# Kernel optimization log

Measured on AMD Instinct MI355X. Metric: run time of the kernel, lower is better.

The kernel has to match this reference:

```python
import jax, jax.numpy as jnp
import numpy as np

SEQ, BATCH, IN, HID = 1024, 512, 128, 256
TAU, DT = 100.0, 20.0
ALPHA = DT / TAU  # 0.2


def setup_inputs() -> dict:
    key = jax.random.key(0)
    k1, k2, k3, k4, k5 = jax.random.split(key, 5)
    # torch Linear default init: U(-1/sqrt(fan_in), 1/sqrt(fan_in))
    bi = 1.0 / np.sqrt(IN)
    bh = 1.0 / np.sqrt(HID)
    return {
        "input": jax.random.normal(k1, (SEQ, BATCH, IN), dtype=jnp.float32),
        "hidden": jnp.zeros((BATCH, HID), dtype=jnp.float32),
        "W_in": jax.random.uniform(k2, (IN, HID), jnp.float32, -bi, bi),
        "b_in": jax.random.uniform(k3, (HID,), jnp.float32, -bi, bi),
        "W_hh": jax.random.uniform(k4, (HID, HID), jnp.float32, -bh, bh),
        "b_hh": jax.random.uniform(k5, (HID,), jnp.float32, -bh, bh),
    }


def reference(input, hidden, W_in, b_in, W_hh, b_hh):
    alpha = jnp.asarray(ALPHA, input.dtype)
    one_minus_alpha = jnp.asarray(1.0 - ALPHA, input.dtype)
    # Precompute input projection for all timesteps in one big GEMM: [S,B,H]
    x_proj = jnp.einsum("sbi,ih->sbh", input, W_in) + b_in + b_hh

    def step(h, xp):
        pre = xp + h @ W_hh
        h_new = one_minus_alpha * h + alpha * jax.nn.relu(pre)
        return h_new, h_new

    h_last, output = jax.lax.scan(step, hidden, x_proj)
    return output, h_last
```

## Files before the change

kernel.cpp:

```cpp
#include <hip/hip_runtime.h>
#include <stdint.h>

#define SEQ 1024
#define BATCH 512
#define IN_DIM 128
#define HID 256

typedef _Float16 f16x8 __attribute__((ext_vector_type(8)));
typedef float f32x4 __attribute__((ext_vector_type(4)));

__device__ __forceinline__ uint16_t f2h(float x) {
    _Float16 h = (_Float16)x;
    return __builtin_bit_cast(uint16_t, h);
}

__launch_bounds__(256, 1)
__global__ void ctrnn_mfma(const float* __restrict__ x,
                           const float* __restrict__ h0,
                           const float* __restrict__ Win,
                           const float* __restrict__ bin,
                           const float* __restrict__ Whh,
                           const float* __restrict__ bhh,
                           float* __restrict__ out) {
    const int tid  = threadIdx.x;
    const int lane = tid & 63;
    const int w    = tid >> 6;
    const int b0   = blockIdx.x * 2;

    const int lr   = lane & 15;
    const int g    = lane >> 4;
    const int arow = lane & 1;

    __shared__ __align__(16) uint16_t HS[2][2][HID];
    __shared__ __align__(16) uint16_t XS[2][2][IN_DIM];

    f16x8 wh[8][4];
    f16x8 wi[4][4];
#pragma unroll
    for (int kt = 0; kt < 8; kt++)
#pragma unroll
        for (int t = 0; t < 4; t++) {
            const int c = w * 64 + t * 16 + lr;
#pragma unroll
            for (int e = 0; e < 8; e++)
                wh[kt][t][e] = (_Float16)Whh[(kt * 32 + g * 8 + e) * HID + c];
        }
#pragma unroll
    for (int kt = 0; kt < 4; kt++)
#pragma unroll
        for (int t = 0; t < 4; t++) {
            const int c = w * 64 + t * 16 + lr;
#pragma unroll
            for (int e = 0; e < 8; e++)
                wi[kt][t][e] = (_Float16)Win[(kt * 32 + g * 8 + e) * HID + c];
        }

    float bias[4], hc0[4], hc1[4];
#pragma unroll
    for (int t = 0; t < 4; t++) {
        const int c = w * 64 + t * 16 + lr;
        bias[t] = bin[c] + bhh[c];
        hc0[t]  = h0[(b0 + 0) * HID + c];
        hc1[t]  = h0[(b0 + 1) * HID + c];
    }

    HS[0][0][tid] = f2h(h0[(b0 + 0) * HID + tid]);
    HS[0][1][tid] = f2h(h0[(b0 + 1) * HID + tid]);
    const int xr = tid >> 7, xc = tid & 127;
    XS[0][xr][xc] = f2h(x[(0 * BATCH + b0 + xr) * IN_DIM + xc]);
    float xv_ready = x[(1 * BATCH + b0 + xr) * IN_DIM + xc];
    float xv_fly   = x[(2 * BATCH + b0 + xr) * IN_DIM + xc];
    __syncthreads();

    for (int s = 0; s < SEQ; s++) {
        const int cur = s & 1;
        const int nxt = cur ^ 1;

        XS[nxt][xr][xc] = f2h(xv_ready);
        xv_ready = xv_fly;
        const int sl = (s + 3 < SEQ) ? (s + 3) : (SEQ - 1);
        xv_fly = x[(sl * BATCH + b0 + xr) * IN_DIM + xc];

        f16x8 ah[8], ax[4];
        const uint16_t* hb = &HS[cur][arow][0];
        const uint16_t* xb = &XS[cur][arow][0];
#pragma unroll
        for (int kt = 0; kt < 8; kt++)
            ah[kt] = *(const f16x8*)&hb[kt * 32 + g * 8];
#pragma unroll
        for (int kt = 0; kt < 4; kt++)
            ax[kt] = *(const f16x8*)&xb[kt * 32 + g * 8];

        f32x4 acc[4];
#pragma unroll
        for (int t = 0; t < 4; t++)
            acc[t] = (f32x4){bias[t], bias[t], bias[t], bias[t]};

#pragma unroll
        for (int kt = 0; kt < 8; kt++)
#pragma unroll
            for (int t = 0; t < 4; t++)
                acc[t] = __builtin_amdgcn_mfma_f32_16x16x32_f16(ah[kt], wh[kt][t], acc[t], 0, 0, 0);
#pragma unroll
        for (int kt = 0; kt < 4; kt++)
#pragma unroll
            for (int t = 0; t < 4; t++)
                acc[t] = __builtin_amdgcn_mfma_f32_16x16x32_f16(ax[kt], wi[kt][t], acc[t], 0, 0, 0);

        float hn0[4], hn1[4];
#pragma unroll
        for (int t = 0; t < 4; t++) {
            hn0[t] = 0.8f * hc0[t] + 0.2f * fmaxf(acc[t][0], 0.0f);
            hn1[t] = 0.8f * hc1[t] + 0.2f * fmaxf(acc[t][1], 0.0f);
            hc0[t] = hn0[t];
            hc1[t] = hn1[t];
        }
        if (lane < 16) {
#pragma unroll
            for (int t = 0; t < 4; t++) {
                const int c = w * 64 + t * 16 + lr;
                HS[nxt][0][c] = f2h(hn0[t]);
                HS[nxt][1][c] = f2h(hn1[t]);
            }
#pragma unroll
            for (int t = 0; t < 4; t++) {
                const int c = w * 64 + t * 16 + lr;
                out[((size_t)s * BATCH + b0 + 0) * HID + c] = hn0[t];
                out[((size_t)s * BATCH + b0 + 1) * HID + c] = hn1[t];
            }
        }
        __syncthreads();
    }

    if (lane < 16) {
        float* hl = out + (size_t)SEQ * BATCH * HID;
#pragma unroll
        for (int t = 0; t < 4; t++) {
            const int c = w * 64 + t * 16 + lr;
            hl[(b0 + 0) * HID + c] = hc0[t];
            hl[(b0 + 1) * HID + c] = hc1[t];
        }
    }
}

extern "C" void kernel_launch(void* const* d_in, const int* in_sizes, int n_in,
                              void* d_out, int out_size, void* d_ws, size_t ws_size,
                              hipStream_t stream) {
    const float* x   = (const float*)d_in[0];
    const float* h0  = (const float*)d_in[1];
    const float* Win = (const float*)d_in[2];
    const float* bin = (const float*)d_in[3];
    const float* Whh = (const float*)d_in[4];
    const float* bhh = (const float*)d_in[5];
    float* out = (float*)d_out;

    ctrnn_mfma<<<BATCH / 2, HID, 0, stream>>>(x, h0, Win, bin, Whh, bhh, out);
}
```

Baseline: 1.476 ms.

## Software-pipeline input projection one step ahead of recurrent MFMA chain

The input-projection MFMAs for step s+1 are now computed during step s into a separate accumulator, so each step's serial critical path holds only the recurrent W_hh MFMAs plus the activation. Staging of x is reworked so 128 threads load float2 and write packed half pairs, with the prefetch distance extended by one step. The loop is unrolled by two with ping-pong accumulators. This costs extra accumulator registers and a more complex buffer rotation.

```diff
diff --git a/kernel.cpp b/kernel.cpp
--- a/kernel.cpp
+++ b/kernel.cpp
@@ -12,6 +12,9 @@
 __device__ __forceinline__ uint16_t f2h(float x) {
     _Float16 h = (_Float16)x;
     return __builtin_bit_cast(uint16_t, h);
+}
+__device__ __forceinline__ uint32_t pack2(float a, float b) {
+    return (uint32_t)f2h(a) | ((uint32_t)f2h(b) << 16);
 }
 
 __launch_bounds__(256, 1)
@@ -66,71 +69,109 @@
 
     HS[0][0][tid] = f2h(h0[(b0 + 0) * HID + tid]);
     HS[0][1][tid] = f2h(h0[(b0 + 1) * HID + tid]);
-    const int xr = tid >> 7, xc = tid & 127;
-    XS[0][xr][xc] = f2h(x[(0 * BATCH + b0 + xr) * IN_DIM + xc]);
-    float xv_ready = x[(1 * BATCH + b0 + xr) * IN_DIM + xc];
-    float xv_fly   = x[(2 * BATCH + b0 + xr) * IN_DIM + xc];
+
+    const bool stg  = tid < 128;
+    const int  srow = (tid >> 6) & 1;
+    const int  sp   = tid & 63;
+    float2 xv_ready = {0.f, 0.f}, xv_fly = {0.f, 0.f};
+    if (stg) {
+        float2 v0 = *(const float2*)&x[((size_t)0 * BATCH + b0 + srow) * IN_DIM + 2 * sp];
+        ((uint32_t*)XS)[(0 * 2 + srow) * 64 + sp] = pack2(v0.x, v0.y);
+        float2 v1 = *(const float2*)&x[((size_t)1 * BATCH + b0 + srow) * IN_DIM + 2 * sp];
+        ((uint32_t*)XS)[(1 * 2 + srow) * 64 + sp] = pack2(v1.x, v1.y);
+        xv_ready = *(const float2*)&x[((size_t)2 * BATCH + b0 + srow) * IN_DIM + 2 * sp];
+        xv_fly   = *(const float2*)&x[((size_t)3 * BATCH + b0 + srow) * IN_DIM + 2 * sp];
+    }
     __syncthreads();
 
-    for (int s = 0; s < SEQ; s++) {
-        const int cur = s & 1;
-        const int nxt = cur ^ 1;
-
-        XS[nxt][xr][xc] = f2h(xv_ready);
-        xv_ready = xv_fly;
-        const int sl = (s + 3 < SEQ) ? (s + 3) : (SEQ - 1);
-        xv_fly = x[(sl * BATCH + b0 + xr) * IN_DIM + xc];
-
-        f16x8 ah[8], ax[4];
-        const uint16_t* hb = &HS[cur][arow][0];
-        const uint16_t* xb = &XS[cur][arow][0];
+    f32x4 xaccA[4], xaccB[4];
+    {
+        f16x8 ax0[4];
+        const uint16_t* xb0 = &XS[0][arow][0];
 #pragma unroll
-        for (int kt = 0; kt < 8; kt++)
-            ah[kt] = *(const f16x8*)&hb[kt * 32 + g * 8];
-#pragma unroll
-        for (int kt = 0; kt < 4; kt++)
-            ax[kt] = *(const f16x8*)&xb[kt * 32 + g * 8];
-
-        f32x4 acc[4];
+    for (int kt = 0; kt < 4; kt++)
+            ax0[kt] = *(const f16x8*)&xb0[kt * 32 + g * 8];
 #pragma unroll
         for (int t = 0; t < 4; t++)
-            acc[t] = (f32x4){bias[t], bias[t], bias[t], bias[t]};
-
-#pragma unroll
-        for (int kt = 0; kt < 8; kt++)
-#pragma unroll
-            for (int t = 0; t < 4; t++)
-                acc[t] = __builtin_amdgcn_mfma_f32_16x16x32_f16(ah[kt], wh[kt][t], acc[t], 0, 0, 0);
+            xaccA[t] = (f32x4){bias[t], bias[t], bias[t], bias[t]};
 #pragma unroll
         for (int kt = 0; kt < 4; kt++)
 #pragma unroll
             for (int t = 0; t < 4; t++)
-                acc[t] = __builtin_amdgcn_mfma_f32_16x16x32_f16(ax[kt], wi[kt][t], acc[t], 0, 0, 0);
+                xaccA[t] = __builtin_amdgcn_mfma_f32_16x16x32_f16(ax0[kt], wi[kt][t], xaccA[t], 0, 0, 0);
+    }
+    __syncthreads();
 
-        float hn0[4], hn1[4];
-#pragma unroll
-        for (int t = 0; t < 4; t++) {
-            hn0[t] = 0.8f * hc0[t] + 0.2f * fmaxf(acc[t][0], 0.0f);
-            hn1[t] = 0.8f * hc1[t] + 0.2f * fmaxf(acc[t][1], 0.0f);
-            hc0[t] = hn0[t];
-            hc1[t] = hn1[t];
-        }
-        if (lane < 16) {
-#pragma unroll
-            for (int t = 0; t < 4; t++) {
-                const int c = w * 64 + t * 16 + lr;
-                HS[nxt][0][c] = f2h(hn0[t]);
-                HS[nxt][1][c] = f2h(hn1[t]);
-            }
-#pragma unroll
-            for (int t = 0; t < 4; t++) {
-                const int c = w * 64 + t * 16 + lr;
-                out[((size_t)s * BATCH + b0 + 0) * HID + c] = hn0[t];
-                out[((size_t)s * BATCH + b0 + 1) * HID + c] = hn1[t];
-            }
-        }
-        __syncthreads();
+#define STEP(S_, ACC_CUR, ACC_NXT)                                                      \
+    {                                                                                   \
+        const int s_   = (S_);                                                          \
+        const int cur_ = s_ & 1;                                                        \
+        const int nxt_ = cur_ ^ 1;                                                      \
+          \
+        f16x8 ax_[4];                                                                   \
+        const uint16_t* xb_ = &XS[nxt_][arow][0];                                       \
+        _Pragma("unroll")                                                               \
+        for (int kt = 0; kt < 4; kt++)                                                  \
+            ax_[kt] = *(const f16x8*)&xb_[kt * 32 + g * 8];                             \
+                                                 \
+        f16x8 ah_[8];                                                                   \
+        const uint16_t* hb_ = &HS[cur_][arow][0];                                       \
+        _Pragma("unroll")                                                               \
+        for (int kt = 0; kt < 8; kt++)                                                  \
+            ah_[kt] = *(const f16x8*)&hb_[kt * 32 + g * 8];                             \
+                                  \
+        if (stg) {                                                                      \
+            ((uint32_t*)XS)[(cur_ * 2 + srow) * 64 + sp] = pack2(xv_ready.x, xv_ready.y); \
+            xv_ready = xv_fly;                                                          \
+            const int sl_ = (s_ + 4 < SEQ) ? (s_ + 4) : (SEQ - 1);                      \
+            xv_fly = *(const float2*)&x[((size_t)sl_ * BATCH + b0 + srow) * IN_DIM + 2 * sp]; \
+        }                                                                               \
+             \
+        _Pragma("unroll")                                                               \
+        for (int t = 0; t < 4; t++)                                                     \
+            ACC_NXT[t] = (f32x4){bias[t], bias[t], bias[t], bias[t]};                   \
+        _Pragma("unroll")                                                               \
+        for (int kt = 0; kt < 4; kt++)                                                  \
+            _Pragma("unroll")                                                           \
+            for (int t = 0; t < 4; t++)                                                 \
+                ACC_NXT[t] = __builtin_amdgcn_mfma_f32_16x16x32_f16(ax_[kt], wi[kt][t], ACC_NXT[t], 0, 0, 0); \
+                                            \
+        _Pragma("unroll")                                                               \
+        for (int kt = 0; kt < 8; kt++)                                                  \
+            _Pragma("unroll")                                                           \
+            for (int t = 0; t < 4; t++)                                                 \
+                ACC_CUR[t] = __builtin_amdgcn_mfma_f32_16x16x32_f16(ah_[kt], wh[kt][t], ACC_CUR[t], 0, 0, 0); \
+                                 \
+        float hn0_[4], hn1_[4];                                                         \
+        _Pragma("unroll")                                                               \
+        for (int t = 0; t < 4; t++) {                                                   \
+            hn0_[t] = 0.8f * hc0[t] + 0.2f * fmaxf(ACC_CUR[t][0], 0.0f);                \
+            hn1_[t] = 0.8f * hc1[t] + 0.2f * fmaxf(ACC_CUR[t][1], 0.0f);                \
+            hc0[t] = hn0_[t];                                                           \
+            hc1[t] = hn1_[t];                                                           \
+        }                                                                               \
+        if (lane < 16) {                                                                \
+            _Pragma("unroll")                                                           \
+            for (int t = 0; t < 4; t++) {                                               \
+                const int c_ = w * 64 + t * 16 + lr;                                    \
+                HS[nxt_][0][c_] = f2h(hn0_[t]);                                         \
+                HS[nxt_][1][c_] = f2h(hn1_[t]);                                         \
+            }                                                                           \
+            _Pragma("unroll")                                                           \
+            for (int t = 0; t < 4; t++) {                                               \
+                const int c_ = w * 64 + t * 16 + lr;                                    \
+                out[((size_t)s_ * BATCH + b0 + 0) * HID + c_] = hn0_[t];                \
+                out[((size_t)s_ * BATCH + b0 + 1) * HID + c_] = hn1_[t];                \
+            }                                                                           \
+        }                                                                               \
+        __syncthreads();                                                                \
     }
+
+    for (int s = 0; s < SEQ; s += 2) {
+        STEP(s,     xaccA, xaccB);
+        STEP(s + 1, xaccB, xaccA);
+    }
+#undef STEP
 
     if (lane < 16) {
         float* hl = out + (size_t)SEQ * BATCH * HID;
```

After: 1.288 ms. 12.8% less time.
